# Kernel optimization log

Hardware: AMD Instinct MI355X
Metric: run time of the kernel (lower is better)

## Reference

```python
import jax, jax.numpy as jnp
import numpy as np

B, S, D_IN, D_OUT, H = 4, 2048, 1024, 1024, 16
HD = D_OUT // H  # head_dim = 64


def setup_inputs() -> dict:
    key = jax.random.key(0)
    ks = jax.random.split(key, 6)
    scale = 1.0 / np.sqrt(D_IN)
    return {
        "x": jax.random.normal(ks[0], (B, S, D_IN), dtype=jnp.float32),
        "Wq": jax.random.normal(ks[1], (D_IN, D_OUT), dtype=jnp.float32) * scale,
        "Wk": jax.random.normal(ks[2], (D_IN, D_OUT), dtype=jnp.float32) * scale,
        "Wv": jax.random.normal(ks[3], (D_IN, D_OUT), dtype=jnp.float32) * scale,
        "Wo": jax.random.normal(ks[4], (D_OUT, D_OUT), dtype=jnp.float32) * (1.0 / np.sqrt(D_OUT)),
        "bo": jax.random.normal(ks[5], (D_OUT,), dtype=jnp.float32) * 0.02,
    }


def reference(x, Wq, Wk, Wv, Wo, bo):
    b, n, _ = x.shape
    h, hd = H, HD
    # projections -> (b, h, n, hd)
    q = (x @ Wq).reshape(b, n, h, hd).transpose(0, 2, 1, 3)
    k = (x @ Wk).reshape(b, n, h, hd).transpose(0, 2, 1, 3)
    v = (x @ Wv).reshape(b, n, h, hd).transpose(0, 2, 1, 3)
    # scores (b, h, n, n) with causal mask then scale (matches original order)
    scores = jnp.einsum("bhqd,bhkd->bhqk", q, k)
    causal = jnp.tril(jnp.ones((n, n), dtype=bool))  # True = keep
    scores = jnp.where(causal, scores, -jnp.inf) / jnp.sqrt(jnp.asarray(hd, x.dtype))
    attn = jax.nn.softmax(scores, axis=-1)
    ctx = jnp.einsum("bhqk,bhkd->bhqd", attn, v)
    ctx = ctx.transpose(0, 2, 1, 3).reshape(b, n, h * hd)
    return ctx @ Wo + bo
```

## Files before the change

### kernel.cpp

```cpp
#include <hip/hip_runtime.h>
#include <hip/hip_bf16.h>
#include <math.h>

typedef __attribute__((ext_vector_type(4))) float f32x4;
typedef __attribute__((ext_vector_type(16))) float f32x16;
typedef __attribute__((ext_vector_type(8))) short bf16x8;
typedef __attribute__((ext_vector_type(4))) unsigned int u32x4;

#define DEV __device__ __forceinline__
#define MFMA16 __builtin_amdgcn_mfma_f32_16x16x32_bf16
#define MFMA32 __builtin_amdgcn_mfma_f32_32x32x16_bf16
#define SBAR __builtin_amdgcn_s_barrier()
#define SCHED0 __builtin_amdgcn_sched_barrier(0)

constexpr int S      = 2048;
constexpr int DMODEL = 1024;
constexpr int HD     = 64;
constexpr int MROWS  = 4 * 2048;

DEV unsigned short f2bf(float f) {
  union { float f; unsigned int u; } v; v.f = f;
  unsigned int u = v.u;
  unsigned int r = u + 0x7fffu + ((u >> 16) & 1u);
  return (unsigned short)(r >> 16);
}

DEV unsigned int pkbf(float lo, float hi) {
  unsigned int r;
  asm("v_cvt_pk_bf16_f32 %0, %1, %2" : "=v"(r) : "v"(lo), "v"(hi));
  return r;
}

DEV float fexp2(float x) { return __builtin_amdgcn_exp2f(x); }

DEV void gload_lds16(const void* g, void* l) {
  __builtin_amdgcn_global_load_lds(
      (const __attribute__((address_space(1))) unsigned int*)g,
      (__attribute__((address_space(3))) unsigned int*)l, 16, 0, 0);
}

__global__ __launch_bounds__(256) void k_conv(const float* __restrict__ in,
                                              unsigned short* __restrict__ out) {
  int i = blockIdx.x * 256 + threadIdx.x;
  float4 v = ((const float4*)in)[i];
  ushort4 o;
  o.x = f2bf(v.x); o.y = f2bf(v.y); o.z = f2bf(v.z); o.w = f2bf(v.w);
  ((ushort4*)out)[i] = o;
}

__global__ __launch_bounds__(256) void k_transpose4(const float* __restrict__ Wq,
                                                    const float* __restrict__ Wk,
                                                    const float* __restrict__ Wv,
                                                    const float* __restrict__ Wo,
                                                    unsigned short* __restrict__ wt,
                                                    unsigned short* __restrict__ wot) {
  __shared__ float tile[32][33];
  const int z = blockIdx.z;
  const float* W = (z == 0) ? Wq : (z == 1) ? Wk : (z == 2) ? Wv : Wo;
  unsigned short* Wt = (z == 3) ? wot : wt + (size_t)z * DMODEL * DMODEL;
  int n0 = blockIdx.x * 32, k0 = blockIdx.y * 32;
  int tx = threadIdx.x, ty = threadIdx.y;
#pragma unroll
  for (int j = 0; j < 4; ++j)
    tile[ty + j * 8][tx] = W[(size_t)(k0 + ty + j * 8) * DMODEL + n0 + tx];
  __syncthreads();
#pragma unroll
  for (int j = 0; j < 4; ++j)
    Wt[(size_t)(n0 + ty + j * 8) * DMODEL + k0 + tx] = f2bf(tile[tx][ty + j * 8]);
}

template<int NBX, int EPI>
__global__ __launch_bounds__(512, 2) void k_gemm8(const unsigned short* __restrict__ A,
                                                  const unsigned short* __restrict__ Bt,
                                                  unsigned short* __restrict__ Qg,
                                                  unsigned short* __restrict__ Kg,
                                                  unsigned short* __restrict__ Vt,
                                                  const float* __restrict__ bo,
                                                  float* __restrict__ out) {
  __shared__ __align__(16) char lds[98304];
  const int tid = threadIdx.x, lane = tid & 63;
  const int wid = tid >> 6, wm = wid >> 1, wn = wid & 1;
  const int lq = lane & 15, lg = lane >> 4;
  const int flat = blockIdx.x;
  const int wg = (flat & 7) * (NBX * 4) + (flat >> 3);
  const int by = wg / NBX, bx = wg % NBX;
  const int m0 = by * 256, n0 = bx * 128;

  auto stage = [&](int kt, int buf) {
    char* dA = lds + buf * 49152;
    char* dB = dA + 32768;
    const unsigned short* gA = A + (size_t)m0 * DMODEL + kt * 64;
    const unsigned short* gB = Bt + (size_t)n0 * DMODEL + kt * 64;
#pragma unroll
    for (int i = 0; i < 4; ++i) {
      int c = tid + i * 512; int r = c >> 3, cc = c & 7;
      gload_lds16(gA + (size_t)r * DMODEL + ((cc ^ (r & 7)) << 3), dA + c * 16);
    }
#pragma unroll
    for (int i = 0; i < 2; ++i) {
      int c = tid + i * 512; int r = c >> 3, cc = c & 7;
      gload_lds16(gB + (size_t)r * DMODEL + ((cc ^ (r & 7)) << 3), dB + c * 16);
    }
  };

  stage(0, 0);
  stage(1, 1);
  SCHED0;
  asm volatile("s_waitcnt vmcnt(6)" ::: "memory");
  SCHED0;
  SBAR;
  SCHED0;

  f32x4 acc[4][4] = {};
#pragma unroll 1
  for (int t = 0; t < 16; ++t) {
    const int cur = t & 1;
    const char* pA = lds + cur * 49152;
    const char* pB = pA + 32768;
    bf16x8 af[4][2], bf[4][2];
#pragma unroll
    for (int kk = 0; kk < 2; ++kk) {
#pragma unroll
      for (int mi = 0; mi < 4; ++mi) {
        int row = wm * 64 + mi * 16 + lq;
        af[mi][kk] = *(const bf16x8*)(pA + row * 128 + ((((kk << 2) + lg) ^ (row & 7)) << 4));
      }
#pragma unroll
      for (int ni = 0; ni < 4; ++ni) {
        int row = wn * 64 + ni * 16 + lq;
        bf[ni][kk] = *(const bf16x8*)(pB + row * 128 + ((((kk << 2) + lg) ^ (row & 7)) << 4));
      }
    }
    asm volatile("s_waitcnt lgkmcnt(0)" ::: "memory");
    SCHED0;
    SBAR;
    SCHED0;
    if (t < 14) stage(t + 2, cur);
    __builtin_amdgcn_s_setprio(1);
#pragma unroll
    for (int kk = 0; kk < 2; ++kk)
#pragma unroll
      for (int mi = 0; mi < 4; ++mi)
#pragma unroll
        for (int ni = 0; ni < 4; ++ni)
          acc[mi][ni] = MFMA16(af[mi][kk], bf[ni][kk], acc[mi][ni], 0, 0, 0);
    __builtin_amdgcn_s_setprio(0);
    SCHED0;
    if (t < 14) {
      asm volatile("s_waitcnt vmcnt(6)" ::: "memory");
    } else if (t == 14) {
      asm volatile("s_waitcnt vmcnt(0)" ::: "memory");
    }
    SCHED0;
    SBAR;
    SCHED0;
  }

  if (EPI == 0) {
#pragma unroll
    for (int mi = 0; mi < 4; ++mi)
#pragma unroll
      for (int ni = 0; ni < 4; ++ni) {
        int n = n0 + wn * 64 + ni * 16 + lq;
        int widx = n >> 10, nn = n & 1023;
        int h = nn >> 6, d = nn & 63;
        int mbase = m0 + wm * 64 + mi * 16 + lg * 4;
        int b_ = mbase >> 11, s_ = mbase & 2047;
        if (widx == 2) {
          ushort4 o;
          o.x = f2bf(acc[mi][ni][0]);
          o.y = f2bf(acc[mi][ni][1]);
          o.z = f2bf(acc[mi][ni][2]);
          o.w = f2bf(acc[mi][ni][3]);
          *(ushort4*)(Vt + ((size_t)((b_ * 16 + h) * 64 + d)) * S + s_) = o;
        } else {
          unsigned short* dst = (widx == 0) ? Qg : Kg;
          float scale = (widx == 0) ? 0.18033688f : 1.0f;
#pragma unroll
          for (int r = 0; r < 4; ++r)
            dst[(size_t)((b_ * 16 + h) * 2048 + s_ + r) * HD + d] = f2bf(acc[mi][ni][r] * scale);
        }
      }
  } else {
#pragma unroll
    for (int mi = 0; mi < 4; ++mi)
#pragma unroll
      for (int ni = 0; ni < 4; ++ni) {
        int n = n0 + wn * 64 + ni * 16 + lq;
        float bv = bo[n];
#pragma unroll
        for (int r = 0; r < 4; ++r) {
          int m = m0 + wm * 64 + mi * 16 + lg * 4 + r;
          out[(size_t)m * DMODEL + n] = acc[mi][ni][r] + bv;
        }
      }
  }
}

__global__ __launch_bounds__(512, 2) void k_attn(const unsigned short* __restrict__ Qg,
                                                 const unsigned short* __restrict__ Kg,
                                                 const unsigned short* __restrict__ Vt,
                                                 unsigned short* __restrict__ Ctx) {
  __shared__ __align__(16) char lds[32768];
  const int f = blockIdx.x;
  const int i4 = f & 255, hi2 = f >> 8;
  const int bh = i4 >> 2, q = i4 & 3;
  const int Qb = hi2 ? (7 - q) : q;
  const int tid = threadIdx.x;
  const int lane = tid & 63, w = tid >> 6;
  const int lq5 = lane & 31, hi = lane >> 5;
  const size_t base = (size_t)bh * (S * HD);
  const int b = bh >> 4, h = bh & 15;
  const int krow = tid >> 3, kcc = tid & 7, scc = kcc ^ (krow & 7);
  const int vd = tid >> 3;
  const int vfd = (vd & 7) ^ ((vd >> 3) & 7);
  const int vscc = (tid & 7) ^ vfd;
  const unsigned short* VtRow = Vt + (size_t)(bh * 64 + vd) * S;

  const int q0w = Qb * 256 + w * 32;
  const int tmax = 4 * Qb + 3;
  const int diag = q0w >> 6;

  bf16x8 qF[4];
#pragma unroll
  for (int dc = 0; dc < 4; ++dc)
    qF[dc] = *(const bf16x8*)(Qg + base + (size_t)(q0w + lq5) * HD + dc * 16 + hi * 8);

  f32x16 o0 = {}, o1 = {};
  float m_run = -INFINITY, l_run = 0.f;

  gload_lds16(Kg + base + (size_t)krow * HD + scc * 8, lds + tid * 16);
  gload_lds16(VtRow + vscc * 8, lds + 16384 + tid * 16);
  __syncthreads();

#pragma unroll 1
  for (int t = 0; t <= tmax; ++t) {
    const int cur = t & 1, nxt = cur ^ 1;
    char* sK  = lds + cur * 8192;
    char* sVT = lds + 16384 + cur * 8192;
    const bool have_next = (t < tmax);
    if (have_next) {
      gload_lds16(Kg + base + (size_t)((t + 1) * 64 + krow) * HD + scc * 8,
                  lds + nxt * 8192 + tid * 16);
      gload_lds16(VtRow + (t + 1) * 64 + vscc * 8,
                  lds + 16384 + nxt * 8192 + tid * 16);
    }
    const bool active = (t <= diag);
    if (active) {
      const bool isdiag = (t == diag);
      const int nkb = (isdiag && !(q0w & 32)) ? 1 : 2;
      f32x16 st0 = {}, st1 = {};
#pragma unroll
      for (int dc = 0; dc < 4; ++dc) {
        int row = lq5;
        bf16x8 a0 = *(const bf16x8*)(sK + row * 128 + (((2 * dc + hi) ^ (row & 7)) << 4));
        st0 = MFMA32(a0, qF[dc], st0, 0, 0, 0);
      }
      if (nkb == 2) {
#pragma unroll
        for (int dc = 0; dc < 4; ++dc) {
          int row = 32 + lq5;
          bf16x8 a1 = *(const bf16x8*)(sK + row * 128 + (((2 * dc + hi) ^ (row & 7)) << 4));
          st1 = MFMA32(a1, qF[dc], st1, 0, 0, 0);
        }
      }
      if (isdiag) {
        int qo = q0w + lq5 - t * 64;
        if (q0w & 32) {
#pragma unroll
          for (int r = 0; r < 16; ++r) {
            int key = 32 + (r & 3) + 8 * (r >> 2) + 4 * hi;
            st1[r] = (key > qo) ? -INFINITY : st1[r];
          }
        } else {
#pragma unroll
          for (int r = 0; r < 16; ++r) {
            int key = (r & 3) + 8 * (r >> 2) + 4 * hi;
            st0[r] = (key > qo) ? -INFINITY : st0[r];
          }
        }
      }
      float mx = st0[0];
#pragma unroll
      for (int r = 1; r < 16; ++r) mx = fmaxf(mx, st0[r]);
      if (nkb == 2) {
#pragma unroll
        for (int r = 0; r < 16; ++r) mx = fmaxf(mx, st1[r]);
      }
      mx = fmaxf(mx, __shfl_xor(mx, 32));
      bool need = !(mx <= m_run + 8.0f);
      if (__any(need)) {
        float mn = fmaxf(m_run, mx);
        float alpha = fexp2(m_run - mn);
        m_run = mn;
        l_run *= alpha;
#pragma unroll
        for (int r = 0; r < 16; ++r) { o0[r] *= alpha; o1[r] *= alpha; }
      }
      float rs[4] = {0.f, 0.f, 0.f, 0.f};
#pragma unroll
      for (int r = 0; r < 16; ++r) {
        float p = fexp2(st0[r] - m_run);
        st0[r] = p;
        rs[r & 3] += p;
      }
      if (nkb == 2) {
#pragma unroll
        for (int r = 0; r < 16; ++r) {
          float p = fexp2(st1[r] - m_run);
          st1[r] = p;
          rs[r & 3] += p;
        }
      }
      float rsum = (rs[0] + rs[1]) + (rs[2] + rs[3]);
      rsum += __shfl_xor(rsum, 32);
      l_run += rsum;
      {
        unsigned int wv[8];
#pragma unroll
        for (int j = 0; j < 8; ++j) wv[j] = pkbf(st0[2 * j], st0[2 * j + 1]);
        asm("v_permlane32_swap_b32 %0, %1" : "+v"(wv[0]), "+v"(wv[2]));
        asm("v_permlane32_swap_b32 %0, %1" : "+v"(wv[1]), "+v"(wv[3]));
        asm("v_permlane32_swap_b32 %0, %1" : "+v"(wv[4]), "+v"(wv[6]));
        asm("v_permlane32_swap_b32 %0, %1" : "+v"(wv[5]), "+v"(wv[7]));
        union { bf16x8 v; unsigned int u[4]; } fa, fb;
        fa.u[0] = wv[0]; fa.u[1] = wv[1]; fa.u[2] = wv[2]; fa.u[3] = wv[3];
        fb.u[0] = wv[4]; fb.u[1] = wv[5]; fb.u[2] = wv[6]; fb.u[3] = wv[7];
#pragma unroll
        for (int kc = 0; kc < 2; ++kc) {
          bf16x8 bp = kc ? fb.v : fa.v;
          {
            int d = lq5, fd = (d & 7) ^ ((d >> 3) & 7);
            bf16x8 av = *(const bf16x8*)(sVT + d * 128 + (((kc * 2 + hi) ^ fd) << 4));
            o0 = MFMA32(av, bp, o0, 0, 0, 0);
          }
          {
            int d = 32 + lq5, fd = (d & 7) ^ ((d >> 3) & 7);
            bf16x8 av = *(const bf16x8*)(sVT + d * 128 + (((kc * 2 + hi) ^ fd) << 4));
            o1 = MFMA32(av, bp, o1, 0, 0, 0);
          }
        }
      }
      if (nkb == 2) {
        unsigned int wv[8];
#pragma unroll
        for (int j = 0; j < 8; ++j) wv[j] = pkbf(st1[2 * j], st1[2 * j + 1]);
        asm("v_permlane32_swap_b32 %0, %1" : "+v"(wv[0]), "+v"(wv[2]));
        asm("v_permlane32_swap_b32 %0, %1" : "+v"(wv[1]), "+v"(wv[3]));
        asm("v_permlane32_swap_b32 %0, %1" : "+v"(wv[4]), "+v"(wv[6]));
        asm("v_permlane32_swap_b32 %0, %1" : "+v"(wv[5]), "+v"(wv[7]));
        union { bf16x8 v; unsigned int u[4]; } fa, fb;
        fa.u[0] = wv[0]; fa.u[1] = wv[1]; fa.u[2] = wv[2]; fa.u[3] = wv[3];
        fb.u[0] = wv[4]; fb.u[1] = wv[5]; fb.u[2] = wv[6]; fb.u[3] = wv[7];
#pragma unroll
        for (int kc = 0; kc < 2; ++kc) {
          bf16x8 bp = kc ? fb.v : fa.v;
          {
            int d = lq5, fd = (d & 7) ^ ((d >> 3) & 7);
            bf16x8 av = *(const bf16x8*)(sVT + d * 128 + ((((2 + kc) * 2 + hi) ^ fd) << 4));
            o0 = MFMA32(av, bp, o0, 0, 0, 0);
          }
          {
            int d = 32 + lq5, fd = (d & 7) ^ ((d >> 3) & 7);
            bf16x8 av = *(const bf16x8*)(sVT + d * 128 + ((((2 + kc) * 2 + hi) ^ fd) << 4));
            o1 = MFMA32(av, bp, o1, 0, 0, 0);
          }
        }
      }
    }
    __syncthreads();
  }

  __syncthreads();
  {
    float inv = 1.0f / l_run;
    char* slice = lds + w * 4096;
#pragma unroll
    for (int db = 0; db < 2; ++db)
#pragma unroll
      for (int j = 0; j < 8; ++j) {
        int d0 = (j & 1) * 2 + (j >> 1) * 8 + 4 * hi + 32 * db;
        float va = (db ? o1[2 * j] : o0[2 * j]) * inv;
        float vb = (db ? o1[2 * j + 1] : o0[2 * j + 1]) * inv;
        *(unsigned int*)(slice + lq5 * 128 + (((d0 >> 3) ^ (lq5 & 7)) << 4) + (d0 & 7) * 2) =
            pkbf(va, vb);
      }
    asm volatile("s_waitcnt lgkmcnt(0)" ::: "memory");
#pragma unroll
    for (int i = 0; i < 4; ++i) {
      int r = lane >> 1, cc = (lane & 1) * 4 + i;
      u32x4 v = *(const u32x4*)(slice + r * 128 + ((cc ^ (r & 7)) << 4));
      *(u32x4*)(Ctx + (size_t)(b * S + q0w + r) * DMODEL + h * HD + cc * 8) = v;
    }
  }
}

extern "C" void kernel_launch(void* const* d_in, const int* in_sizes, int n_in,
                              void* d_out, int out_size, void* d_ws, size_t ws_size,
                              hipStream_t stream) {
  const float* x  = (const float*)d_in[0];
  const float* Wq = (const float*)d_in[1];
  const float* Wk = (const float*)d_in[2];
  const float* Wv = (const float*)d_in[3];
  const float* Wo = (const float*)d_in[4];
  const float* bo = (const float*)d_in[5];
  float* out = (float*)d_out;

  char* p = (char*)d_ws;
  unsigned short* xb  = (unsigned short*)p; p += (size_t)MROWS * DMODEL * 2;
  unsigned short* wt  = (unsigned short*)p; p += (size_t)3 * DMODEL * DMODEL * 2;
  unsigned short* wot = (unsigned short*)p; p += (size_t)DMODEL * DMODEL * 2;
  unsigned short* qg  = (unsigned short*)p; p += (size_t)MROWS * DMODEL * 2;
  unsigned short* kg  = (unsigned short*)p; p += (size_t)MROWS * DMODEL * 2;
  unsigned short* vt  = (unsigned short*)p; p += (size_t)MROWS * DMODEL * 2;
  unsigned short* ctx = (unsigned short*)p; p += (size_t)MROWS * DMODEL * 2;

  k_conv<<<(MROWS * DMODEL) / 1024, 256, 0, stream>>>(x, xb);
  k_transpose4<<<dim3(32, 32, 4), dim3(32, 8), 0, stream>>>(Wq, Wk, Wv, Wo, wt, wot);
  k_gemm8<24, 0><<<768, 512, 0, stream>>>(xb, wt, qg, kg, vt, nullptr, nullptr);
  k_attn<<<512, 512, 0, stream>>>(qg, kg, vt, ctx);
  k_gemm8<8, 1><<<256, 512, 0, stream>>>(ctx, wot, nullptr, nullptr, nullptr, bo, out);
}
```

Measured before the change: 166.1 us.

## Load GEMM B operand directly to registers and triple-buffer A in LDS

The GEMM kernel stops staging the B tile through LDS. Each wave now loads its B fragments straight from global memory into registers, double-buffered across k-steps. The A tile moves to a three-slot LDS ring, so the next stage is issued before the current tile's MFMAs and one barrier per k-step is dropped. The intent is to cut LDS traffic and barrier stalls, at the cost of more VGPRs for B and uncoalesced-ish per-wave global loads of B.

```diff
diff --git a/kernel.cpp b/kernel.cpp
--- a/kernel.cpp
+++ b/kernel.cpp
@@ -68,6 +68,36 @@
   for (int j = 0; j < 4; ++j)
     Wt[(size_t)(n0 + ty + j * 8) * DMODEL + k0 + tx] = f2bf(tile[tx][ty + j * 8]);
 }
+
+#define LOADB(kt, Ba)                                                                  \
+  do {                                                                                 \
+    Ba[0] = *(const bf16x8*)(gBbase + 0 * 16 * (size_t)DMODEL + (kt) * 64 + 0);        \
+    Ba[1] = *(const bf16x8*)(gBbase + 0 * 16 * (size_t)DMODEL + (kt) * 64 + 32);       \
+    Ba[2] = *(const bf16x8*)(gBbase + 1 * 16 * (size_t)DMODEL + (kt) * 64 + 0);        \
+    Ba[3] = *(const bf16x8*)(gBbase + 1 * 16 * (size_t)DMODEL + (kt) * 64 + 32);       \
+    Ba[4] = *(const bf16x8*)(gBbase + 2 * 16 * (size_t)DMODEL + (kt) * 64 + 0);        \
+    Ba[5] = *(const bf16x8*)(gBbase + 2 * 16 * (size_t)DMODEL + (kt) * 64 + 32);       \
+    Ba[6] = *(const bf16x8*)(gBbase + 3 * 16 * (size_t)DMODEL + (kt) * 64 + 0);        \
+    Ba[7] = *(const bf16x8*)(gBbase + 3 * 16 * (size_t)DMODEL + (kt) * 64 + 32);       \
+  } while (0)
+
+#define TILE(bcur, Ba)                                                                 \
+  do {                                                                                 \
+    const char* pA = lds + (bcur) * 32768;                                             \
+    _Pragma("unroll") for (int kk = 0; kk < 2; ++kk) {                                 \
+      bf16x8 af[4];                                                                    \
+      _Pragma("unroll") for (int mi = 0; mi < 4; ++mi) {                               \
+        int row = wm * 64 + mi * 16 + lq;                                              \
+        af[mi] = *(const bf16x8*)(pA + row * 128 +                                     \
+                                  ((((kk << 2) + lg) ^ (row & 7)) << 4));              \
+      }                                                                                \
+      __builtin_amdgcn_s_setprio(1);                                                   \
+      _Pragma("unroll") for (int mi = 0; mi < 4; ++mi)                                 \
+        _Pragma("unroll") for (int ni = 0; ni < 4; ++ni)                               \
+          acc[mi][ni] = MFMA16(af[mi], Ba[ni * 2 + kk], acc[mi][ni], 0, 0, 0);         \
+      __builtin_amdgcn_s_setprio(0);                                                   \
+    }                                                                                  \
+  } while (0)
 
 template<int NBX, int EPI>
 __global__ __launch_bounds__(512, 2) void k_gemm8(const unsigned short* __restrict__ A,
@@ -86,74 +116,61 @@
   const int by = wg / NBX, bx = wg % NBX;
   const int m0 = by * 256, n0 = bx * 128;
 
-  auto stage = [&](int kt, int buf) {
-    char* dA = lds + buf * 49152;
-    char* dB = dA + 32768;
+  const unsigned short* gBbase = Bt + (size_t)(n0 + wn * 64 + lq) * DMODEL + lg * 8;
+
+  auto stageA = [&](int kt, int buf) {
+    char* dA = lds + buf * 32768;
     const unsigned short* gA = A + (size_t)m0 * DMODEL + kt * 64;
-    const unsigned short* gB = Bt + (size_t)n0 * DMODEL + kt * 64;
 #pragma unroll
     for (int i = 0; i < 4; ++i) {
       int c = tid + i * 512; int r = c >> 3, cc = c & 7;
       gload_lds16(gA + (size_t)r * DMODEL + ((cc ^ (r & 7)) << 3), dA + c * 16);
     }
-#pragma unroll
-    for (int i = 0; i < 2; ++i) {
-      int c = tid + i * 512; int r = c >> 3, cc = c & 7;
-      gload_lds16(gB + (size_t)r * DMODEL + ((cc ^ (r & 7)) << 3), dB + c * 16);
-    }
   };
 
-  stage(0, 0);
-  stage(1, 1);
+  bf16x8 Be[8], Bo[8];
+  LOADB(0, Be);
+  stageA(0, 0);
+  stageA(1, 1);
+  LOADB(1, Bo);
   SCHED0;
-  asm volatile("s_waitcnt vmcnt(6)" ::: "memory");
+  asm volatile("s_waitcnt vmcnt(12)" ::: "memory");
   SCHED0;
   SBAR;
   SCHED0;
 
   f32x4 acc[4][4] = {};
+  int bcur = 0, bth = 2;
 #pragma unroll 1
-  for (int t = 0; t < 16; ++t) {
-    const int cur = t & 1;
-    const char* pA = lds + cur * 49152;
-    const char* pB = pA + 32768;
-    bf16x8 af[4][2], bf[4][2];
-#pragma unroll
-    for (int kk = 0; kk < 2; ++kk) {
-#pragma unroll
-      for (int mi = 0; mi < 4; ++mi) {
-        int row = wm * 64 + mi * 16 + lq;
-        af[mi][kk] = *(const bf16x8*)(pA + row * 128 + ((((kk << 2) + lg) ^ (row & 7)) << 4));
-      }
-#pragma unroll
-      for (int ni = 0; ni < 4; ++ni) {
-        int row = wn * 64 + ni * 16 + lq;
-        bf[ni][kk] = *(const bf16x8*)(pB + row * 128 + ((((kk << 2) + lg) ^ (row & 7)) << 4));
-      }
-    }
-    asm volatile("s_waitcnt lgkmcnt(0)" ::: "memory");
+  for (int it = 0; it < 8; ++it) {
+    const int t = 2 * it;
+    if (t < 14) stageA(t + 2, bth);
+    TILE(bcur, Be);
+    if (t < 14) LOADB(t + 2, Be);
+    SCHED0;
+    if (t < 14) {
+      asm volatile("s_waitcnt vmcnt(12)" ::: "memory");
+    } else {
+      asm volatile("s_waitcnt vmcnt(0)" ::: "memory");
+    }
     SCHED0;
     SBAR;
     SCHED0;
-    if (t < 14) stage(t + 2, cur);
-    __builtin_amdgcn_s_setprio(1);
-#pragma unroll
-    for (int kk = 0; kk < 2; ++kk)
-#pragma unroll
-      for (int mi = 0; mi < 4; ++mi)
-#pragma unroll
-        for (int ni = 0; ni < 4; ++ni)
-          acc[mi][ni] = MFMA16(af[mi][kk], bf[ni][kk], acc[mi][ni], 0, 0, 0);
-    __builtin_amdgcn_s_setprio(0);
+    bcur = (bcur + 1 == 3) ? 0 : bcur + 1;
+    bth  = (bth + 1 == 3) ? 0 : bth + 1;
+    const int t1 = t + 1;
+    if (t1 < 14) stageA(t1 + 2, bth);
+    TILE(bcur, Bo);
+    if (t1 < 14) LOADB(t1 + 2, Bo);
     SCHED0;
-    if (t < 14) {
-      asm volatile("s_waitcnt vmcnt(6)" ::: "memory");
-    } else if (t == 14) {
-      asm volatile("s_waitcnt vmcnt(0)" ::: "memory");
-    }
-    SCHED0;
-    SBAR;
-    SCHED0;
+    if (t1 < 15) {
+      asm volatile("s_waitcnt vmcnt(12)" ::: "memory");
+      SCHED0;
+      SBAR;
+      SCHED0;
+    }
+    bcur = (bcur + 1 == 3) ? 0 : bcur + 1;
+    bth  = (bth + 1 == 3) ? 0 : bth + 1;
   }
 
   if (EPI == 0) {
```

After: 235.2 us. 1.42x slower.

## Triple-buffer GEMM LDS and split each k-tile into two interleaved half-stages

Applied to the files above, without the earlier changes.

The bf16 GEMM moves from two LDS buffers to three (144 KB). Each 64-wide k-tile is now processed as two 32-wide halves, and half of the next-next tile's global-to-LDS loads are issued alongside each half. This aims to overlap global loads, LDS reads and MFMA work more finely, and to drop the barrier that sat between the LDS reads and the prefetch. The cost is higher LDS use and extra barriers per iteration, and the GEMM is only part of the total runtime.

```diff
diff --git a/kernel.cpp b/kernel.cpp
--- a/kernel.cpp
+++ b/kernel.cpp
@@ -77,7 +77,7 @@
                                                   unsigned short* __restrict__ Vt,
                                                   const float* __restrict__ bo,
                                                   float* __restrict__ out) {
-  __shared__ __align__(16) char lds[98304];
+  __shared__ __align__(16) char lds[147456];
   const int tid = threadIdx.x, lane = tid & 63;
   const int wid = tid >> 6, wm = wid >> 1, wn = wid & 1;
   const int lq = lane & 15, lg = lane >> 4;
@@ -86,7 +86,7 @@
   const int by = wg / NBX, bx = wg % NBX;
   const int m0 = by * 256, n0 = bx * 128;
 
-  auto stage = [&](int kt, int buf) {
+  auto stageFull = [&](int kt, int buf) {
     char* dA = lds + buf * 49152;
     char* dB = dA + 32768;
     const unsigned short* gA = A + (size_t)m0 * DMODEL + kt * 64;
@@ -102,9 +102,24 @@
       gload_lds16(gB + (size_t)r * DMODEL + ((cc ^ (r & 7)) << 3), dB + c * 16);
     }
   };
-
-  stage(0, 0);
-  stage(1, 1);
+  auto stageHalf = [&](int kt, int buf, int half) {
+    char* dA = lds + buf * 49152;
+    char* dB = dA + 32768;
+    const unsigned short* gA = A + (size_t)m0 * DMODEL + kt * 64;
+    const unsigned short* gB = Bt + (size_t)n0 * DMODEL + kt * 64;
+#pragma unroll
+    for (int i = 0; i < 2; ++i) {
+      int c = tid + (2 * half + i) * 512; int r = c >> 3, cc = c & 7;
+      gload_lds16(gA + (size_t)r * DMODEL + ((cc ^ (r & 7)) << 3), dA + c * 16);
+    }
+    {
+      int c = tid + half * 512; int r = c >> 3, cc = c & 7;
+      gload_lds16(gB + (size_t)r * DMODEL + ((cc ^ (r & 7)) << 3), dB + c * 16);
+    }
+  };
+
+  stageFull(0, 0);
+  stageFull(1, 1);
   SCHED0;
   asm volatile("s_waitcnt vmcnt(6)" ::: "memory");
   SCHED0;
@@ -112,48 +127,72 @@
   SCHED0;
 
   f32x4 acc[4][4] = {};
+  int bcur = 0, bth = 2;
 #pragma unroll 1
   for (int t = 0; t < 16; ++t) {
-    const int cur = t & 1;
-    const char* pA = lds + cur * 49152;
+    const char* pA = lds + bcur * 49152;
     const char* pB = pA + 32768;
-    bf16x8 af[4][2], bf[4][2];
-#pragma unroll
-    for (int kk = 0; kk < 2; ++kk) {
+    {
+      bf16x8 af[4], bfr[4];
 #pragma unroll
       for (int mi = 0; mi < 4; ++mi) {
         int row = wm * 64 + mi * 16 + lq;
-        af[mi][kk] = *(const bf16x8*)(pA + row * 128 + ((((kk << 2) + lg) ^ (row & 7)) << 4));
+        af[mi] = *(const bf16x8*)(pA + row * 128 + ((lg ^ (row & 7)) << 4));
       }
 #pragma unroll
       for (int ni = 0; ni < 4; ++ni) {
         int row = wn * 64 + ni * 16 + lq;
-        bf[ni][kk] = *(const bf16x8*)(pB + row * 128 + ((((kk << 2) + lg) ^ (row & 7)) << 4));
-      }
-    }
-    asm volatile("s_waitcnt lgkmcnt(0)" ::: "memory");
-    SCHED0;
-    SBAR;
-    SCHED0;
-    if (t < 14) stage(t + 2, cur);
-    __builtin_amdgcn_s_setprio(1);
-#pragma unroll
-    for (int kk = 0; kk < 2; ++kk)
+        bfr[ni] = *(const bf16x8*)(pB + row * 128 + ((lg ^ (row & 7)) << 4));
+      }
+      if (t < 14) stageHalf(t + 2, bth, 0);
+      SBAR;
+      asm volatile("s_waitcnt lgkmcnt(0)" ::: "memory");
+      SCHED0;
+      __builtin_amdgcn_s_setprio(1);
 #pragma unroll
       for (int mi = 0; mi < 4; ++mi)
 #pragma unroll
         for (int ni = 0; ni < 4; ++ni)
-          acc[mi][ni] = MFMA16(af[mi][kk], bf[ni][kk], acc[mi][ni], 0, 0, 0);
-    __builtin_amdgcn_s_setprio(0);
-    SCHED0;
+          acc[mi][ni] = MFMA16(af[mi], bfr[ni], acc[mi][ni], 0, 0, 0);
+      __builtin_amdgcn_s_setprio(0);
+      SCHED0;
+    }
+    {
+      bf16x8 af[4], bfr[4];
+#pragma unroll
+      for (int mi = 0; mi < 4; ++mi) {
+        int row = wm * 64 + mi * 16 + lq;
+        af[mi] = *(const bf16x8*)(pA + row * 128 + (((4 + lg) ^ (row & 7)) << 4));
+      }
+#pragma unroll
+      for (int ni = 0; ni < 4; ++ni) {
+        int row = wn * 64 + ni * 16 + lq;
+        bfr[ni] = *(const bf16x8*)(pB + row * 128 + (((4 + lg) ^ (row & 7)) << 4));
+      }
+      if (t < 14) stageHalf(t + 2, bth, 1);
+      SBAR;
+      asm volatile("s_waitcnt lgkmcnt(0)" ::: "memory");
+      SCHED0;
+      __builtin_amdgcn_s_setprio(1);
+#pragma unroll
+      for (int mi = 0; mi < 4; ++mi)
+#pragma unroll
+        for (int ni = 0; ni < 4; ++ni)
+          acc[mi][ni] = MFMA16(af[mi], bfr[ni], acc[mi][ni], 0, 0, 0);
+      __builtin_amdgcn_s_setprio(0);
+      SCHED0;
+    }
     if (t < 14) {
       asm volatile("s_waitcnt vmcnt(6)" ::: "memory");
     } else if (t == 14) {
       asm volatile("s_waitcnt vmcnt(0)" ::: "memory");
     }
     SCHED0;
-    SBAR;
+    if (t < 15) SBAR;
     SCHED0;
+    int nb = (bcur + 1 == 3) ? 0 : bcur + 1;
+    int nt = (bth + 1 == 3) ? 0 : bth + 1;
+    bcur = nb; bth = nt;
   }
 
   if (EPI == 0) {
```

After: 168.7 us. About the same (+1.6%).
